# Kernel optimization log

Hardware: AMD Instinct MI355X
Metric: run time of the kernel (lower is better)

The kernel has to match this reference:

```python
import jax, jax.numpy as jnp
import numpy as np

B, N, D, H, S = 32, 8192, 64, 128, 16
ITERS, TAU = 3, 0.1


def _ln(x, g, b):
    m = x.mean(-1, keepdims=True)
    v = ((x - m) ** 2).mean(-1, keepdims=True)
    return (x - m) / jnp.sqrt(v + 1e-5) * g + b


def setup_inputs() -> dict:
    key = jax.random.key(0)
    ks = jax.random.split(key, 20)
    nrm = lambda k, shp, s: jax.random.normal(k, shp, jnp.float32) * s
    return {
        'x': nrm(ks[0], (B, N, D), 1.0),
        'w1': nrm(ks[1], (D, H), D ** -0.5), 'b1': jnp.zeros((H,), jnp.float32),
        'ln1_g': jnp.ones((H,), jnp.float32), 'ln1_b': jnp.zeros((H,), jnp.float32),
        'w2': nrm(ks[2], (H, H), H ** -0.5), 'b2': jnp.zeros((H,), jnp.float32),
        'ln2_g': jnp.ones((H,), jnp.float32), 'ln2_b': jnp.zeros((H,), jnp.float32),
        'slot_mu': nrm(ks[3], (1, S, H), 0.1),
        'gru_wi': nrm(ks[4], (3 * H, H), H ** -0.5), 'gru_wh': nrm(ks[5], (3 * H, H), H ** -0.5),
        'gru_bi': jnp.zeros((3 * H,), jnp.float32), 'gru_bh': jnp.zeros((3 * H,), jnp.float32),
        'mlp_w1': nrm(ks[6], (H, H), H ** -0.5), 'mlp_b1': jnp.zeros((H,), jnp.float32),
        'mlp_w2': nrm(ks[7], (H, H), H ** -0.5), 'mlp_b2': jnp.zeros((H,), jnp.float32),
        'norm_g': jnp.ones((H,), jnp.float32), 'norm_b': jnp.zeros((H,), jnp.float32),
    }


def reference(x, w1, b1, ln1_g, ln1_b, w2, b2, ln2_g, ln2_b, slot_mu,
              gru_wi, gru_wh, gru_bi, gru_bh, mlp_w1, mlp_b1, mlp_w2, mlp_b2,
              norm_g, norm_b):
    Bb = x.shape[0]
    h = jax.nn.gelu(_ln(x @ w1 + b1, ln1_g, ln1_b), approximate=False)
    feats = _ln(h @ w2 + b2, ln2_g, ln2_b)              # [B,N,H]
    slots = jnp.broadcast_to(slot_mu, (Bb, S, H))
    f2 = jnp.sum(feats * feats, -1)                      # [B,N]
    attn = None
    for _ in range(ITERS):
        s2 = jnp.sum(slots * slots, -1)                  # [B,S]
        sf = jnp.einsum('bsh,bnh->bsn', slots, feats)
        dist_sq = -(s2[:, :, None] - 2.0 * sf + f2[:, None, :])  # -||s-f||^2
        attn = jax.nn.softmax(dist_sq / TAU, axis=1)     # softmax over slots
        w = attn / (attn.sum(2, keepdims=True) + 1e-8)
        updates = jnp.einsum('bsn,bnh->bsh', w, feats)
        # GRUCell (PyTorch gate order: r, z, n)
        gi = updates @ gru_wi.T + gru_bi
        gh = slots @ gru_wh.T + gru_bh
        ir, iz, inn = jnp.split(gi, 3, -1)
        hr, hz, hn = jnp.split(gh, 3, -1)
        r = jax.nn.sigmoid(ir + hr)
        z = jax.nn.sigmoid(iz + hz)
        n = jnp.tanh(inn + r * hn)
        new = (1.0 - z) * n + z * slots
        mlp_out = jax.nn.gelu(_ln(new, norm_g, norm_b) @ mlp_w1 + mlp_b1, approximate=False) @ mlp_w2 + mlp_b2
        slots = new + 0.2 * mlp_out
    return (slots, attn)
```

## Files before the change

kernel.cpp:

```cpp
#include <hip/hip_runtime.h>
#include <cstddef>
#include <cstdint>

#define B_ 32
#define N_ 8192
#define D_ 64
#define H_ 128
#define S_ 16
#define L2SCALE 14.426950408889634f

typedef unsigned short ushort_t;
typedef __attribute__((ext_vector_type(8))) short short8;
typedef __attribute__((ext_vector_type(4))) float f32x4;

#define NCHUNK 512
#define NBLK   (N_ / NCHUNK)
#define PSTRIDE 520

__device__ __forceinline__ float gelu_exact(float x){
    return 0.5f * x * (1.0f + erff(x * 0.70710678118654752f));
}
__device__ __forceinline__ ushort_t f2bf(float f){
    unsigned u = __float_as_uint(f);
    unsigned r = (u + 0x7FFF + ((u >> 16) & 1)) >> 16;
    return (ushort_t)r;
}
__device__ __forceinline__ float bf2f(ushort_t h){
    return __uint_as_float(((unsigned)h) << 16);
}

__global__ __launch_bounds__(256) void feats_kernel(
    const float* __restrict__ x, const float* __restrict__ w1, const float* __restrict__ b1,
    const float* __restrict__ ln1g, const float* __restrict__ ln1b,
    const float* __restrict__ w2g, const float* __restrict__ b2,
    const float* __restrict__ ln2g, const float* __restrict__ ln2b,
    ushort_t* __restrict__ f_hi, ushort_t* __restrict__ f_lo)
{
    __shared__ float smem[12544];
    float* xs  = smem;
    float* w1s = smem + 4352;
    float* hs  = smem;
    float* w2s = smem + 8448;

    const int tid  = threadIdx.x;
    const int row0 = blockIdx.x * 64;
    const int c0   = (tid & 15) * 8;
    const int r0   = (tid >> 4) * 4;

    for (int i = tid; i < 1024; i += 256){
        int r = i >> 4, c4 = i & 15;
        float4 v = *(const float4*)(x + (size_t)(row0 + r) * 64 + c4 * 4);
        *(float4*)(xs + r * 68 + c4 * 4) = v;
    }
    for (int i = tid; i < 2048; i += 256)
        ((float4*)w1s)[i] = ((const float4*)w1)[i];
    __syncthreads();

    float acc[4][8];
    #pragma unroll
    for (int i=0;i<4;++i){
        #pragma unroll
        for (int j=0;j<8;++j) acc[i][j]=0.f;
    }
    #pragma unroll 4
    for (int d = 0; d < 64; ++d){
        float4 bv0 = *(const float4*)(w1s + d*128 + c0);
        float4 bv1 = *(const float4*)(w1s + d*128 + c0 + 4);
        float bv[8] = {bv0.x,bv0.y,bv0.z,bv0.w,bv1.x,bv1.y,bv1.z,bv1.w};
        float av[4];
        #pragma unroll
        for (int i=0;i<4;++i) av[i] = xs[(r0+i)*68 + d];
        #pragma unroll
        for (int i=0;i<4;++i){
            #pragma unroll
            for (int j=0;j<8;++j) acc[i][j] += av[i]*bv[j];
        }
    }

    float4 bb0 = *(const float4*)(b1 + c0),   bb1 = *(const float4*)(b1 + c0 + 4);
    float4 gg0 = *(const float4*)(ln1g + c0), gg1 = *(const float4*)(ln1g + c0 + 4);
    float4 be0 = *(const float4*)(ln1b + c0), be1 = *(const float4*)(ln1b + c0 + 4);
    float bia[8] = {bb0.x,bb0.y,bb0.z,bb0.w,bb1.x,bb1.y,bb1.z,bb1.w};
    float gam[8] = {gg0.x,gg0.y,gg0.z,gg0.w,gg1.x,gg1.y,gg1.z,gg1.w};
    float bet[8] = {be0.x,be0.y,be0.z,be0.w,be1.x,be1.y,be1.z,be1.w};

    float hrow[4][8];
    #pragma unroll
    for (int i=0;i<4;++i){
        float v[8]; float s1=0.f, sq=0.f;
        #pragma unroll
        for (int j=0;j<8;++j){ v[j] = acc[i][j] + bia[j]; s1 += v[j]; sq += v[j]*v[j]; }
        #pragma unroll
        for (int m=1; m<16; m<<=1){ s1 += __shfl_xor(s1, m); sq += __shfl_xor(sq, m); }
        float mean = s1 * (1.0f/128.0f);
        float var  = sq * (1.0f/128.0f) - mean*mean;
        float rs   = 1.0f / sqrtf(var + 1e-5f);
        #pragma unroll
        for (int j=0;j<8;++j){
            float t = (v[j]-mean)*rs*gam[j] + bet[j];
            hrow[i][j] = gelu_exact(t);
        }
    }
    __syncthreads();
    #pragma unroll
    for (int i=0;i<4;++i){
        *(float4*)(hs + (r0+i)*132 + c0)     = make_float4(hrow[i][0],hrow[i][1],hrow[i][2],hrow[i][3]);
        *(float4*)(hs + (r0+i)*132 + c0 + 4) = make_float4(hrow[i][4],hrow[i][5],hrow[i][6],hrow[i][7]);
    }

    float acc2[4][8];
    #pragma unroll
    for (int i=0;i<4;++i){
        #pragma unroll
        for (int j=0;j<8;++j) acc2[i][j]=0.f;
    }
    for (int ck = 0; ck < 4; ++ck){
        __syncthreads();
        for (int i = tid; i < 1024; i += 256)
            ((float4*)w2s)[i] = ((const float4*)w2g)[ck*1024 + i];
        __syncthreads();
        #pragma unroll 4
        for (int k=0;k<32;++k){
            float4 bv0 = *(const float4*)(w2s + k*128 + c0);
            float4 bv1 = *(const float4*)(w2s + k*128 + c0 + 4);
            float bv[8] = {bv0.x,bv0.y,bv0.z,bv0.w,bv1.x,bv1.y,bv1.z,bv1.w};
            int kk = ck*32 + k;
            float av[4];
            #pragma unroll
            for (int i=0;i<4;++i) av[i] = hs[(r0+i)*132 + kk];
            #pragma unroll
            for (int i=0;i<4;++i){
                #pragma unroll
                for (int j=0;j<8;++j) acc2[i][j] += av[i]*bv[j];
            }
        }
    }

    float4 cb0 = *(const float4*)(b2 + c0),   cb1 = *(const float4*)(b2 + c0 + 4);
    float4 cg0 = *(const float4*)(ln2g + c0), cg1 = *(const float4*)(ln2g + c0 + 4);
    float4 ce0 = *(const float4*)(ln2b + c0), ce1 = *(const float4*)(ln2b + c0 + 4);
    float bia2[8] = {cb0.x,cb0.y,cb0.z,cb0.w,cb1.x,cb1.y,cb1.z,cb1.w};
    float gam2[8] = {cg0.x,cg0.y,cg0.z,cg0.w,cg1.x,cg1.y,cg1.z,cg1.w};
    float bet2[8] = {ce0.x,ce0.y,ce0.z,ce0.w,ce1.x,ce1.y,ce1.z,ce1.w};

    #pragma unroll
    for (int i=0;i<4;++i){
        float v[8]; float s1=0.f, sq=0.f;
        #pragma unroll
        for (int j=0;j<8;++j){ v[j] = acc2[i][j] + bia2[j]; s1 += v[j]; sq += v[j]*v[j]; }
        #pragma unroll
        for (int m=1; m<16; m<<=1){ s1 += __shfl_xor(s1, m); sq += __shfl_xor(sq, m); }
        float mean = s1 * (1.0f/128.0f);
        float var  = sq * (1.0f/128.0f) - mean*mean;
        float rs   = 1.0f / sqrtf(var + 1e-5f);
        short8 vhi, vlo;
        #pragma unroll
        for (int j=0;j<8;++j){
            float o = (v[j]-mean)*rs*gam2[j] + bet2[j];
            ushort_t hi = f2bf(o);
            float lo = o - bf2f(hi);
            vhi[j] = (short)hi;
            vlo[j] = (short)f2bf(lo);
        }
        size_t off = (size_t)(row0 + r0 + i)*128 + c0;
        *(short8*)(f_hi + off) = vhi;
        *(short8*)(f_lo + off) = vlo;
    }
}

__global__ void init_slots(const float* __restrict__ mu, float* __restrict__ slots){
    int i = blockIdx.x * 256 + threadIdx.x;
    slots[i] = mu[i & 2047];
}

__global__ __launch_bounds__(512, 4) void attn_kernel(
    const ushort_t* __restrict__ f_hi, const ushort_t* __restrict__ f_lo,
    const float* __restrict__ slots,
    float* __restrict__ pn, float* __restrict__ pd,
    float* __restrict__ attn_out, const int write_attn)
{
    __shared__ ushort_t P_hi[16*PSTRIDE];
    __shared__ ushort_t P_lo[16*PSTRIDE];
    __shared__ float    s2buf[16];
    __shared__ float    den_red[16];

    const int tid  = threadIdx.x;
    const int w    = tid >> 6;
    const int l    = tid & 63;
    const int ln   = l & 15;
    const int quad = l >> 4;
    const int b    = blockIdx.x >> 4;
    const int nc   = blockIdx.x & 15;
    const int n0   = nc * NCHUNK;

    if (tid < 16) den_red[tid] = 0.f;

    short8 sa_hi[4], sa_lo[4];
    float q2 = 0.f;
    {
        const float* sp = slots + ((size_t)(b*16 + ln))*128 + quad*8;
        #pragma unroll
        for (int ks=0; ks<4; ++ks){
            float4 v0 = *(const float4*)(sp + ks*32);
            float4 v1 = *(const float4*)(sp + ks*32 + 4);
            float v[8] = {v0.x,v0.y,v0.z,v0.w,v1.x,v1.y,v1.z,v1.w};
            #pragma unroll
            for (int j=0;j<8;++j){
                q2 += v[j]*v[j];
                ushort_t hi = f2bf(v[j]);
                float lo = v[j] - bf2f(hi);
                sa_hi[ks][j] = (short)hi;
                sa_lo[ks][j] = (short)f2bf(lo);
            }
        }
    }
    q2 += __shfl_xor(q2, 16);
    q2 += __shfl_xor(q2, 32);
    if (tid < 16) s2buf[tid] = q2;
    __syncthreads();

    float s2v[4];
    #pragma unroll
    for (int r=0;r<4;++r) s2v[r] = s2buf[quad*4 + r];

    float den_acc[4] = {0.f,0.f,0.f,0.f};
    const size_t fbase = (size_t)b*N_ + n0;

    #pragma unroll
    for (int t2=0; t2<4; ++t2){
        const int t  = w*4 + t2;
        const int nl = t*16 + ln;
        const size_t rowoff = (fbase + nl) * 128;

        short8 fh[4], fl[4];
        #pragma unroll
        for (int ks=0; ks<4; ++ks){
            fh[ks] = *(const short8*)(f_hi + rowoff + ks*32 + quad*8);
            fl[ks] = *(const short8*)(f_lo + rowoff + ks*32 + quad*8);
        }

        f32x4 d = {0.f,0.f,0.f,0.f};
        #pragma unroll
        for (int ks=0;ks<4;++ks) d = __builtin_amdgcn_mfma_f32_16x16x32_bf16(sa_hi[ks], fh[ks], d, 0,0,0);
        #pragma unroll
        for (int ks=0;ks<4;++ks) d = __builtin_amdgcn_mfma_f32_16x16x32_bf16(sa_hi[ks], fl[ks], d, 0,0,0);
        #pragma unroll
        for (int ks=0;ks<4;++ks) d = __builtin_amdgcn_mfma_f32_16x16x32_bf16(sa_lo[ks], fh[ks], d, 0,0,0);

        float L[4];
        #pragma unroll
        for (int r=0;r<4;++r) L[r] = (2.f*d[r] - s2v[r]) * L2SCALE;
        float mx = fmaxf(fmaxf(L[0],L[1]), fmaxf(L[2],L[3]));
        mx = fmaxf(mx, __shfl_xor(mx, 16));
        mx = fmaxf(mx, __shfl_xor(mx, 32));
        float e[4];
        float z = 0.f;
        #pragma unroll
        for (int r=0;r<4;++r){ e[r] = exp2f(L[r] - mx); z += e[r]; }
        z += __shfl_xor(z, 16);
        z += __shfl_xor(z, 32);
        float rz = 1.f / z;
        #pragma unroll
        for (int r=0;r<4;++r){
            float p = e[r] * rz;
            den_acc[r] += p;
            if (write_attn)
                attn_out[((size_t)(b*16 + quad*4 + r))*N_ + n0 + nl] = p;
            ushort_t ph = f2bf(p);
            float plr = p - bf2f(ph);
            P_hi[(quad*4+r)*PSTRIDE + nl] = ph;
            P_lo[(quad*4+r)*PSTRIDE + nl] = f2bf(plr);
        }
    }

    #pragma unroll
    for (int m=1; m<16; m<<=1){
        #pragma unroll
        for (int r=0;r<4;++r) den_acc[r] += __shfl_xor(den_acc[r], m);
    }
    if (ln == 0){
        #pragma unroll
        for (int r=0;r<4;++r) atomicAdd(&den_red[quad*4 + r], den_acc[r]);
    }
    __syncthreads();

    f32x4 dacc = {0.f,0.f,0.f,0.f};
    #pragma unroll 2
    for (int ks=0; ks<16; ++ks){
        short8 pah = *(const short8*)(&P_hi[ln*PSTRIDE + ks*32 + quad*8]);
        short8 pal = *(const short8*)(&P_lo[ln*PSTRIDE + ks*32 + quad*8]);
        short8 fbh, fbl;
        #pragma unroll
        for (int j=0;j<8;++j){
            size_t go = (fbase + (size_t)(ks*32 + quad*8 + j))*128 + w*16 + ln;
            fbh[j] = (short)f_hi[go];
            fbl[j] = (short)f_lo[go];
        }
        dacc = __builtin_amdgcn_mfma_f32_16x16x32_bf16(pah, fbh, dacc, 0,0,0);
        dacc = __builtin_amdgcn_mfma_f32_16x16x32_bf16(pal, fbh, dacc, 0,0,0);
        dacc = __builtin_amdgcn_mfma_f32_16x16x32_bf16(pah, fbl, dacc, 0,0,0);
    }
    {
        float* dst = pn + (size_t)blockIdx.x * 2048;
        #pragma unroll
        for (int r=0;r<4;++r)
            dst[(quad*4+r)*128 + w*16 + ln] = dacc[r];
    }
    if (tid < 16) pd[blockIdx.x*16 + tid] = den_red[tid];
}

__global__ __launch_bounds__(256) void update_kernel(
    const float* __restrict__ pn, const float* __restrict__ pd,
    float* __restrict__ slots,
    const float* __restrict__ gwi, const float* __restrict__ gwh,
    const float* __restrict__ gbi, const float* __restrict__ gbh,
    const float* __restrict__ mw1, const float* __restrict__ mb1,
    const float* __restrict__ mw2, const float* __restrict__ mb2,
    const float* __restrict__ ng, const float* __restrict__ nbv,
    float* __restrict__ out_slots, const int write_out)
{
    __shared__ float us[512], sl[512], gbuf[3072], nbuf[512], lnb[512], qb[512];
    const int tid  = threadIdx.x;
    const int row0 = blockIdx.x * 4;

    for (int i = tid; i < 512; i += 256){
        int r = i >> 7, h = i & 127;
        int grow = row0 + r;
        int bb = grow >> 4, ss = grow & 15;
        float sum = 0.f, dv = 0.f;
        #pragma unroll 4
        for (int c = 0; c < NBLK; ++c)
            sum += pn[((size_t)(bb*NBLK + c))*2048 + ss*128 + h];
        #pragma unroll
        for (int c = 0; c < NBLK; ++c)
            dv += pd[(bb*NBLK + c)*16 + ss];
        us[i] = sum / (dv + 1e-8f);
        sl[i] = slots[(size_t)grow*128 + h];
    }
    __syncthreads();

    for (int idx = tid; idx < 3072; idx += 256){
        int which = idx >= 1536;
        int rem   = idx - which*1536;
        int r     = rem / 384;
        int o     = rem - r*384;
        const float* W   = which ? gwh : gwi;
        const float* bb  = which ? gbh : gbi;
        const float* src = (which ? sl : us) + r*128;
        float a = bb[o];
        const float4* Wr = (const float4*)(W + (size_t)o*128);
        #pragma unroll 8
        for (int k4=0;k4<32;++k4){
            float4 wv = Wr[k4];
            float4 sv = *(const float4*)(src + 4*k4);
            a += sv.x*wv.x + sv.y*wv.y + sv.z*wv.z + sv.w*wv.w;
        }
        gbuf[idx] = a;
    }
    __syncthreads();

    for (int i = tid; i < 512; i += 256){
        int r = i >> 7, h = i & 127;
        float ir  = gbuf[r*384 + h];
        float iz  = gbuf[r*384 + 128 + h];
        float in_ = gbuf[r*384 + 256 + h];
        float hr  = gbuf[1536 + r*384 + h];
        float hz  = gbuf[1536 + r*384 + 128 + h];
        float hn  = gbuf[1536 + r*384 + 256 + h];
        float rg = 1.f/(1.f + expf(-(ir+hr)));
        float zg = 1.f/(1.f + expf(-(iz+hz)));
        float nn = tanhf(in_ + rg*hn);
        nbuf[i] = (1.f - zg)*nn + zg*sl[i];
    }
    __syncthreads();

    {
        int wv = tid >> 6, ll = tid & 63;
        float v0 = nbuf[wv*128 + ll], v1 = nbuf[wv*128 + 64 + ll];
        float s1 = v0 + v1, sq = v0*v0 + v1*v1;
        #pragma unroll
        for (int m=1; m<64; m<<=1){ s1 += __shfl_xor(s1,m); sq += __shfl_xor(sq,m); }
        float mean = s1*(1.f/128.f), var = sq*(1.f/128.f) - mean*mean;
        float rs = 1.f/sqrtf(var + 1e-5f);
        lnb[wv*128 + ll]      = (v0-mean)*rs*ng[ll] + nbv[ll];
        lnb[wv*128 + 64 + ll] = (v1-mean)*rs*ng[64+ll] + nbv[64+ll];
    }
    __syncthreads();

    for (int i = tid; i < 512; i += 256){
        int r = i >> 7, o = i & 127;
        float a = mb1[o];
        const float* lr = lnb + r*128;
        #pragma unroll 8
        for (int k=0;k<128;++k) a += lr[k] * mw1[(size_t)k*128 + o];
        qb[i] = gelu_exact(a);
    }
    __syncthreads();

    for (int i = tid; i < 512; i += 256){
        int r = i >> 7, h = i & 127;
        float a = mb2[h];
        const float* qr = qb + r*128;
        #pragma unroll 8
        for (int k=0;k<128;++k) a += qr[k] * mw2[(size_t)k*128 + h];
        float ov = nbuf[i] + 0.2f*a;
        int grow = row0 + r;
        slots[(size_t)grow*128 + h] = ov;
        if (write_out) out_slots[(size_t)grow*128 + h] = ov;
    }
}

extern "C" void kernel_launch(void* const* d_in, const int* in_sizes, int n_in,
                              void* d_out, int out_size, void* d_ws, size_t ws_size,
                              hipStream_t stream)
{
    const float* x    = (const float*)d_in[0];
    const float* w1   = (const float*)d_in[1];
    const float* b1   = (const float*)d_in[2];
    const float* ln1g = (const float*)d_in[3];
    const float* ln1b = (const float*)d_in[4];
    const float* w2   = (const float*)d_in[5];
    const float* b2   = (const float*)d_in[6];
    const float* ln2g = (const float*)d_in[7];
    const float* ln2b = (const float*)d_in[8];
    const float* smu  = (const float*)d_in[9];
    const float* gwi  = (const float*)d_in[10];
    const float* gwh  = (const float*)d_in[11];
    const float* gbi  = (const float*)d_in[12];
    const float* gbh  = (const float*)d_in[13];
    const float* mw1  = (const float*)d_in[14];
    const float* mb1  = (const float*)d_in[15];
    const float* mw2  = (const float*)d_in[16];
    const float* mb2  = (const float*)d_in[17];
    const float* ng   = (const float*)d_in[18];
    const float* nbv  = (const float*)d_in[19];

    float* out_slots = (float*)d_out;
    float* out_attn  = (float*)d_out + (size_t)B_*S_*H_;

    ushort_t* f_hi = (ushort_t*)d_ws;
    ushort_t* f_lo = f_hi + (size_t)B_*N_*H_;
    float* slots = (float*)(f_lo + (size_t)B_*N_*H_);
    float* pn    = slots + B_*S_*H_;
    float* pd    = pn + (size_t)(B_*NBLK)*2048;

    feats_kernel<<<dim3(4096), dim3(256), 0, stream>>>(
        x, w1, b1, ln1g, ln1b, w2, b2, ln2g, ln2b, f_hi, f_lo);
    init_slots<<<dim3(256), dim3(256), 0, stream>>>(smu, slots);

    for (int it = 0; it < 3; ++it){
        attn_kernel<<<dim3(B_*NBLK), dim3(512), 0, stream>>>(
            f_hi, f_lo, slots, pn, pd, out_attn, (it==2) ? 1 : 0);
        update_kernel<<<dim3(128), dim3(256), 0, stream>>>(
            pn, pd, slots, gwi, gwh, gbi, gbh, mw1, mb1, mw2, mb2, ng, nbv,
            out_slots, (it==2) ? 1 : 0);
    }
}
```

Baseline: 651.5 us.

## Split feature MLP into two MFMA bf16x3 GEMM kernels with in-place intermediate

Measured after the change: 658.7 us. Within noise of the previous version (+1.1%).

```diff
diff --git a/kernel.cpp b/kernel.cpp
--- a/kernel.cpp
+++ b/kernel.cpp
@@ -17,6 +17,9 @@
 #define NBLK   (N_ / NCHUNK)
 #define PSTRIDE 520
 
+#define W1T_STR 72
+#define W2T_STR 136
+
 __device__ __forceinline__ float gelu_exact(float x){
     return 0.5f * x * (1.0f + erff(x * 0.70710678118654752f));
 }
@@ -29,142 +32,192 @@
     return __uint_as_float(((unsigned)h) << 16);
 }
 
-__global__ __launch_bounds__(256) void feats_kernel(
+__global__ __launch_bounds__(256) void gemm1_kernel(
     const float* __restrict__ x, const float* __restrict__ w1, const float* __restrict__ b1,
     const float* __restrict__ ln1g, const float* __restrict__ ln1b,
-    const float* __restrict__ w2g, const float* __restrict__ b2,
-    const float* __restrict__ ln2g, const float* __restrict__ ln2b,
-    ushort_t* __restrict__ f_hi, ushort_t* __restrict__ f_lo)
+    ushort_t* __restrict__ h_hi, ushort_t* __restrict__ h_lo)
 {
-    __shared__ float smem[12544];
-    float* xs  = smem;
-    float* w1s = smem + 4352;
-    float* hs  = smem;
-    float* w2s = smem + 8448;
+    __shared__ ushort_t w1t_hi[128*W1T_STR];
+    __shared__ ushort_t w1t_lo[128*W1T_STR];
 
     const int tid  = threadIdx.x;
-    const int row0 = blockIdx.x * 64;
-    const int c0   = (tid & 15) * 8;
-    const int r0   = (tid >> 4) * 4;
-
-    for (int i = tid; i < 1024; i += 256){
-        int r = i >> 4, c4 = i & 15;
-        float4 v = *(const float4*)(x + (size_t)(row0 + r) * 64 + c4 * 4);
-        *(float4*)(xs + r * 68 + c4 * 4) = v;
-    }
-    for (int i = tid; i < 2048; i += 256)
-        ((float4*)w1s)[i] = ((const float4*)w1)[i];
-    __syncthreads();
-
-    float acc[4][8];
-    #pragma unroll
-    for (int i=0;i<4;++i){
-        #pragma unroll
-        for (int j=0;j<8;++j) acc[i][j]=0.f;
-    }
-    #pragma unroll 4
-    for (int d = 0; d < 64; ++d){
-        float4 bv0 = *(const float4*)(w1s + d*128 + c0);
-        float4 bv1 = *(const float4*)(w1s + d*128 + c0 + 4);
-        float bv[8] = {bv0.x,bv0.y,bv0.z,bv0.w,bv1.x,bv1.y,bv1.z,bv1.w};
-        float av[4];
-        #pragma unroll
-        for (int i=0;i<4;++i) av[i] = xs[(r0+i)*68 + d];
-        #pragma unroll
-        for (int i=0;i<4;++i){
-            #pragma unroll
-            for (int j=0;j<8;++j) acc[i][j] += av[i]*bv[j];
-        }
-    }
-
-    float4 bb0 = *(const float4*)(b1 + c0),   bb1 = *(const float4*)(b1 + c0 + 4);
-    float4 gg0 = *(const float4*)(ln1g + c0), gg1 = *(const float4*)(ln1g + c0 + 4);
-    float4 be0 = *(const float4*)(ln1b + c0), be1 = *(const float4*)(ln1b + c0 + 4);
-    float bia[8] = {bb0.x,bb0.y,bb0.z,bb0.w,bb1.x,bb1.y,bb1.z,bb1.w};
-    float gam[8] = {gg0.x,gg0.y,gg0.z,gg0.w,gg1.x,gg1.y,gg1.z,gg1.w};
-    float bet[8] = {be0.x,be0.y,be0.z,be0.w,be1.x,be1.y,be1.z,be1.w};
-
-    float hrow[4][8];
-    #pragma unroll
-    for (int i=0;i<4;++i){
-        float v[8]; float s1=0.f, sq=0.f;
-        #pragma unroll
-        for (int j=0;j<8;++j){ v[j] = acc[i][j] + bia[j]; s1 += v[j]; sq += v[j]*v[j]; }
-        #pragma unroll
-        for (int m=1; m<16; m<<=1){ s1 += __shfl_xor(s1, m); sq += __shfl_xor(sq, m); }
-        float mean = s1 * (1.0f/128.0f);
-        float var  = sq * (1.0f/128.0f) - mean*mean;
-        float rs   = 1.0f / sqrtf(var + 1e-5f);
-        #pragma unroll
-        for (int j=0;j<8;++j){
-            float t = (v[j]-mean)*rs*gam[j] + bet[j];
-            hrow[i][j] = gelu_exact(t);
-        }
-    }
-    __syncthreads();
-    #pragma unroll
-    for (int i=0;i<4;++i){
-        *(float4*)(hs + (r0+i)*132 + c0)     = make_float4(hrow[i][0],hrow[i][1],hrow[i][2],hrow[i][3]);
-        *(float4*)(hs + (r0+i)*132 + c0 + 4) = make_float4(hrow[i][4],hrow[i][5],hrow[i][6],hrow[i][7]);
-    }
-
-    float acc2[4][8];
-    #pragma unroll
-    for (int i=0;i<4;++i){
-        #pragma unroll
-        for (int j=0;j<8;++j) acc2[i][j]=0.f;
-    }
-    for (int ck = 0; ck < 4; ++ck){
-        __syncthreads();
-        for (int i = tid; i < 1024; i += 256)
-            ((float4*)w2s)[i] = ((const float4*)w2g)[ck*1024 + i];
-        __syncthreads();
-        #pragma unroll 4
-        for (int k=0;k<32;++k){
-            float4 bv0 = *(const float4*)(w2s + k*128 + c0);
-            float4 bv1 = *(const float4*)(w2s + k*128 + c0 + 4);
-            float bv[8] = {bv0.x,bv0.y,bv0.z,bv0.w,bv1.x,bv1.y,bv1.z,bv1.w};
-            int kk = ck*32 + k;
-            float av[4];
-            #pragma unroll
-            for (int i=0;i<4;++i) av[i] = hs[(r0+i)*132 + kk];
-            #pragma unroll
-            for (int i=0;i<4;++i){
+    const int w    = tid >> 6;
+    const int l    = tid & 63;
+    const int ln   = l & 15;
+    const int quad = l >> 4;
+    const size_t n0 = (size_t)blockIdx.x * 256;
+
+    for (int i = tid; i < 8192; i += 256){
+        int k = i >> 7, hc = i & 127;
+        float v = w1[i];
+        ushort_t hi = f2bf(v);
+        w1t_hi[hc*W1T_STR + k] = hi;
+        w1t_lo[hc*W1T_STR + k] = f2bf(v - bf2f(hi));
+    }
+    __syncthreads();
+
+    for (int tt = 0; tt < 4; ++tt){
+        const size_t row = n0 + (size_t)(w*4 + tt)*16 + ln;
+        const float* xr = x + row*64;
+
+        short8 bxh[2], bxl[2];
+        #pragma unroll
+        for (int kc = 0; kc < 2; ++kc){
+            float4 a0 = *(const float4*)(xr + kc*32 + quad*8);
+            float4 a1 = *(const float4*)(xr + kc*32 + quad*8 + 4);
+            float v[8] = {a0.x,a0.y,a0.z,a0.w,a1.x,a1.y,a1.z,a1.w};
+            #pragma unroll
+            for (int j=0;j<8;++j){
+                ushort_t hi = f2bf(v[j]);
+                bxh[kc][j] = (short)hi;
+                bxl[kc][j] = (short)f2bf(v[j] - bf2f(hi));
+            }
+        }
+
+        f32x4 acc[8];
+        #pragma unroll
+        for (int ht=0;ht<8;++ht) acc[ht] = (f32x4){0.f,0.f,0.f,0.f};
+
+        #pragma unroll
+        for (int ht = 0; ht < 8; ++ht){
+            #pragma unroll
+            for (int kc = 0; kc < 2; ++kc){
+                short8 ah = *(const short8*)&w1t_hi[(ht*16+ln)*W1T_STR + kc*32 + quad*8];
+                short8 al = *(const short8*)&w1t_lo[(ht*16+ln)*W1T_STR + kc*32 + quad*8];
+                acc[ht] = __builtin_amdgcn_mfma_f32_16x16x32_bf16(ah, bxh[kc], acc[ht], 0,0,0);
+                acc[ht] = __builtin_amdgcn_mfma_f32_16x16x32_bf16(ah, bxl[kc], acc[ht], 0,0,0);
+                acc[ht] = __builtin_amdgcn_mfma_f32_16x16x32_bf16(al, bxh[kc], acc[ht], 0,0,0);
+            }
+        }
+
+        float vals[8][4];
+        float s1 = 0.f, sq = 0.f;
+        #pragma unroll
+        for (int ht=0;ht<8;++ht){
+            float bb[4]; *(float4*)bb = *(const float4*)(b1 + ht*16 + quad*4);
+            #pragma unroll
+            for (int r=0;r<4;++r){
+                float v = acc[ht][r] + bb[r];
+                vals[ht][r] = v; s1 += v; sq += v*v;
+            }
+        }
+        s1 += __shfl_xor(s1,16); s1 += __shfl_xor(s1,32);
+        sq += __shfl_xor(sq,16); sq += __shfl_xor(sq,32);
+        float mean = s1 * (1.f/128.f);
+        float var  = sq * (1.f/128.f) - mean*mean;
+        float rs   = 1.f / sqrtf(var + 1e-5f);
+
+        #pragma unroll
+        for (int ht=0;ht<8;++ht){
+            float gg[4]; *(float4*)gg = *(const float4*)(ln1g + ht*16 + quad*4);
+            float be[4]; *(float4*)be = *(const float4*)(ln1b + ht*16 + quad*4);
+            ushort_t oh[4], ol[4];
+            #pragma unroll
+            for (int r=0;r<4;++r){
+                float t  = (vals[ht][r]-mean)*rs*gg[r] + be[r];
+                float ge = gelu_exact(t);
+                ushort_t hi = f2bf(ge);
+                oh[r] = hi;
+                ol[r] = f2bf(ge - bf2f(hi));
+            }
+            size_t off = row*128 + ht*16 + quad*4;
+            *(ushort4*)(h_hi + off) = make_ushort4(oh[0],oh[1],oh[2],oh[3]);
+            *(ushort4*)(h_lo + off) = make_ushort4(ol[0],ol[1],ol[2],ol[3]);
+        }
+    }
+}
+
+__global__ __launch_bounds__(256) void gemm2_kernel(
+    ushort_t* __restrict__ buf_hi, ushort_t* __restrict__ buf_lo,
+    const float* __restrict__ w2, const float* __restrict__ b2,
+    const float* __restrict__ ln2g, const float* __restrict__ ln2b)
+{
+    __shared__ ushort_t w2t_hi[128*W2T_STR];
+    __shared__ ushort_t w2t_lo[128*W2T_STR];
+
+    const int tid  = threadIdx.x;
+    const int w    = tid >> 6;
+    const int l    = tid & 63;
+    const int ln   = l & 15;
+    const int quad = l >> 4;
+    const size_t n0 = (size_t)blockIdx.x * 256;
+
+    for (int i = tid; i < 16384; i += 256){
+        int k = i >> 7, hc = i & 127;
+        float v = w2[i];
+        ushort_t hi = f2bf(v);
+        w2t_hi[hc*W2T_STR + k] = hi;
+        w2t_lo[hc*W2T_STR + k] = f2bf(v - bf2f(hi));
+    }
+    __syncthreads();
+
+    for (int g = 0; g < 2; ++g){
+        size_t row[2];
+        row[0] = n0 + (size_t)(w*4 + g*2 + 0)*16 + ln;
+        row[1] = n0 + (size_t)(w*4 + g*2 + 1)*16 + ln;
+
+        f32x4 acc[2][8];
+        #pragma unroll
+        for (int t2=0;t2<2;++t2)
+            #pragma unroll
+            for (int ht=0;ht<8;++ht) acc[t2][ht] = (f32x4){0.f,0.f,0.f,0.f};
+
+        #pragma unroll
+        for (int kc = 0; kc < 4; ++kc){
+            short8 bh[2], bl[2];
+            #pragma unroll
+            for (int t2=0;t2<2;++t2){
+                bh[t2] = *(const short8*)(buf_hi + row[t2]*128 + kc*32 + quad*8);
+                bl[t2] = *(const short8*)(buf_lo + row[t2]*128 + kc*32 + quad*8);
+            }
+            #pragma unroll
+            for (int ht = 0; ht < 8; ++ht){
+                short8 ah = *(const short8*)&w2t_hi[(ht*16+ln)*W2T_STR + kc*32 + quad*8];
+                short8 al = *(const short8*)&w2t_lo[(ht*16+ln)*W2T_STR + kc*32 + quad*8];
                 #pragma unroll
-                for (int j=0;j<8;++j) acc2[i][j] += av[i]*bv[j];
-            }
-        }
-    }
-
-    float4 cb0 = *(const float4*)(b2 + c0),   cb1 = *(const float4*)(b2 + c0 + 4);
-    float4 cg0 = *(const float4*)(ln2g + c0), cg1 = *(const float4*)(ln2g + c0 + 4);
-    float4 ce0 = *(const float4*)(ln2b + c0), ce1 = *(const float4*)(ln2b + c0 + 4);
-    float bia2[8] = {cb0.x,cb0.y,cb0.z,cb0.w,cb1.x,cb1.y,cb1.z,cb1.w};
-    float gam2[8] = {cg0.x,cg0.y,cg0.z,cg0.w,cg1.x,cg1.y,cg1.z,cg1.w};
-    float bet2[8] = {ce0.x,ce0.y,ce0.z,ce0.w,ce1.x,ce1.y,ce1.z,ce1.w};
-
-    #pragma unroll
-    for (int i=0;i<4;++i){
-        float v[8]; float s1=0.f, sq=0.f;
-        #pragma unroll
-        for (int j=0;j<8;++j){ v[j] = acc2[i][j] + bia2[j]; s1 += v[j]; sq += v[j]*v[j]; }
-        #pragma unroll
-        for (int m=1; m<16; m<<=1){ s1 += __shfl_xor(s1, m); sq += __shfl_xor(sq, m); }
-        float mean = s1 * (1.0f/128.0f);
-        float var  = sq * (1.0f/128.0f) - mean*mean;
-        float rs   = 1.0f / sqrtf(var + 1e-5f);
-        short8 vhi, vlo;
-        #pragma unroll
-        for (int j=0;j<8;++j){
-            float o = (v[j]-mean)*rs*gam2[j] + bet2[j];
-            ushort_t hi = f2bf(o);
-            float lo = o - bf2f(hi);
-            vhi[j] = (short)hi;
-            vlo[j] = (short)f2bf(lo);
-        }
-        size_t off = (size_t)(row0 + r0 + i)*128 + c0;
-        *(short8*)(f_hi + off) = vhi;
-        *(short8*)(f_lo + off) = vlo;
+                for (int t2=0;t2<2;++t2){
+                    acc[t2][ht] = __builtin_amdgcn_mfma_f32_16x16x32_bf16(ah, bh[t2], acc[t2][ht], 0,0,0);
+                    acc[t2][ht] = __builtin_amdgcn_mfma_f32_16x16x32_bf16(ah, bl[t2], acc[t2][ht], 0,0,0);
+                    acc[t2][ht] = __builtin_amdgcn_mfma_f32_16x16x32_bf16(al, bh[t2], acc[t2][ht], 0,0,0);
+                }
+            }
+        }
+
+        #pragma unroll
+        for (int t2=0;t2<2;++t2){
+            float vals[8][4];
+            float s1 = 0.f, sq = 0.f;
+            #pragma unroll
+            for (int ht=0;ht<8;++ht){
+                float bb[4]; *(float4*)bb = *(const float4*)(b2 + ht*16 + quad*4);
+                #pragma unroll
+                for (int r=0;r<4;++r){
+                    float v = acc[t2][ht][r] + bb[r];
+                    vals[ht][r] = v; s1 += v; sq += v*v;
+                }
+            }
+            s1 += __shfl_xor(s1,16); s1 += __shfl_xor(s1,32);
+            sq += __shfl_xor(sq,16); sq += __shfl_xor(sq,32);
+            float mean = s1 * (1.f/128.f);
+            float var  = sq * (1.f/128.f) - mean*mean;
+            float rs   = 1.f / sqrtf(var + 1e-5f);
+            #pragma unroll
+            for (int ht=0;ht<8;++ht){
+                float gg[4]; *(float4*)gg = *(const float4*)(ln2g + ht*16 + quad*4);
+                float be[4]; *(float4*)be = *(const float4*)(ln2b + ht*16 + quad*4);
+                ushort_t oh[4], ol[4];
+                #pragma unroll
+                for (int r=0;r<4;++r){
+                    float o = (vals[ht][r]-mean)*rs*gg[r] + be[r];
+                    ushort_t hi = f2bf(o);
+                    oh[r] = hi;
+                    ol[r] = f2bf(o - bf2f(hi));
+                }
+                size_t off = row[t2]*128 + ht*16 + quad*4;
+                *(ushort4*)(buf_hi + off) = make_ushort4(oh[0],oh[1],oh[2],oh[3]);
+                *(ushort4*)(buf_lo + off) = make_ushort4(ol[0],ol[1],ol[2],ol[3]);
+            }
+        }
     }
 }
 
@@ -173,7 +226,7 @@
     slots[i] = mu[i & 2047];
 }
 
-__global__ __launch_bounds__(512, 4) void attn_kernel(
+__global__ __launch_bounds__(512, 2) void attn_kernel(
     const ushort_t* __restrict__ f_hi, const ushort_t* __restrict__ f_lo,
     const float* __restrict__ slots,
     float* __restrict__ pn, float* __restrict__ pd,
@@ -438,19 +491,21 @@
     float* out_slots = (float*)d_out;
     float* out_attn  = (float*)d_out + (size_t)B_*S_*H_;
 
-    ushort_t* f_hi = (ushort_t*)d_ws;
-    ushort_t* f_lo = f_hi + (size_t)B_*N_*H_;
-    float* slots = (float*)(f_lo + (size_t)B_*N_*H_);
+    ushort_t* buf_hi = (ushort_t*)d_ws;
+    ushort_t* buf_lo = buf_hi + (size_t)B_*N_*H_;
+    float* slots = (float*)(buf_lo + (size_t)B_*N_*H_);
     float* pn    = slots + B_*S_*H_;
     float* pd    = pn + (size_t)(B_*NBLK)*2048;
 
-    feats_kernel<<<dim3(4096), dim3(256), 0, stream>>>(
-        x, w1, b1, ln1g, ln1b, w2, b2, ln2g, ln2b, f_hi, f_lo);
+    gemm1_kernel<<<dim3(1024), dim3(256), 0, stream>>>(
+        x, w1, b1, ln1g, ln1b, buf_hi, buf_lo);
+    gemm2_kernel<<<dim3(1024), dim3(256), 0, stream>>>(
+        buf_hi, buf_lo, w2, b2, ln2g, ln2b);
     init_slots<<<dim3(256), dim3(256), 0, stream>>>(smu, slots);
 
     for (int it = 0; it < 3; ++it){
         attn_kernel<<<dim3(B_*NBLK), dim3(512), 0, stream>>>(
-            f_hi, f_lo, slots, pn, pd, out_attn, (it==2) ? 1 : 0);
+            buf_hi, buf_lo, slots, pn, pd, out_attn, (it==2) ? 1 : 0);
         update_kernel<<<dim3(128), dim3(256), 0, stream>>>(
             pn, pd, slots, gwi, gwh, gbi, gbh, mw1, mb1, mw2, mb2, ng, nbv,
             out_slots, (it==2) ? 1 : 0);
```
